# Performance work log

Hardware: AMD Instinct MI355X
Metric: run time of the kernel (lower is better)

## Reference

```python
import jax, jax.numpy as jnp
import numpy as np
from jax import lax

B, S, D = 4, 128, 256
POOL = 3


def conv_block(x, w, b, stride, pool_k):
    # x: (N, Cin, H, W), w: (Cout, Cin, kh, kw)
    y = lax.conv_general_dilated(
        x, w, window_strides=(stride, stride), padding='VALID',
        dimension_numbers=('NCHW', 'OIHW', 'NCHW'))
    y = y + b[None, :, None, None]
    y = jax.nn.gelu(y, approximate=False)  # torch GELU default is exact
    # MaxPool2d(kernel_size=pool_k) -> stride = pool_k, VALID
    y = lax.reduce_window(y, -jnp.inf, lax.max,
                          (1, 1, pool_k, pool_k), (1, 1, pool_k, pool_k), 'VALID')
    return y


def setup_inputs() -> dict:
    key = jax.random.key(0)
    ks = jax.random.split(key, 8)
    token_features = jax.random.normal(ks[0], (B, S, D), dtype=jnp.float32)
    type_embedds = jax.random.normal(ks[1], (B, S, D), dtype=jnp.float32)
    # Conv2dFeatures(depth=3, num_channels=16, start_kernel=3, start_stride=2, pool_kernel=3)
    w1 = jax.random.normal(ks[2], (16, 1, 3, 3), dtype=jnp.float32) * 0.1
    b1 = jax.random.normal(ks[3], (16,), dtype=jnp.float32) * 0.01
    w2 = jax.random.normal(ks[4], (32, 16, 3, 3), dtype=jnp.float32) * 0.05
    b2 = jax.random.normal(ks[5], (32,), dtype=jnp.float32) * 0.01
    w3 = jax.random.normal(ks[6], (32, 32, 3, 3), dtype=jnp.float32) * 0.05
    b3 = jax.random.normal(ks[7], (32,), dtype=jnp.float32) * 0.01
    return dict(token_features=token_features, type_embedds=type_embedds,
                w1=w1, b1=b1, w2=w2, b2=b2, w3=w3, b3=b3)


def reference(token_features, type_embedds, w1, b1, w2, b2, w3, b3):
    b, s, d = type_embedds.shape
    # Outter2dFusion: fused[n,s,i,j] = type_embedds[n,s,i] * token_features[n,s,j]
    fused = jnp.einsum('bsi,bsj->bsij', type_embedds, token_features)
    # Conv stack applied per seq position with in_channels=1 == one batched conv
    x = fused.reshape(b * s, 1, d, d)
    x = conv_block(x, w1, b1, stride=2, pool_k=POOL)
    x = conv_block(x, w2, b2, stride=1, pool_k=POOL)
    x = conv_block(x, w3, b3, stride=1, pool_k=POOL)
    # Dropout is identity in eval mode
    return x.reshape(b, s, -1)
```

## Files before the change

### kernel.cpp

```cpp
#include <hip/hip_runtime.h>
#include <math.h>


#define NIMG 512

__device__ __forceinline__ float gelu_exact(float x) {
    return 0.5f * x * (1.0f + erff(x * 0.70710678118654752f));
}

__device__ __forceinline__ float pool_gelu(float vmin, float vmax) {
    return fmaxf(gelu_exact(vmin), gelu_exact(vmax));
}

__global__ __launch_bounds__(256) void k1_fused(const float* __restrict__ tok,
                                                const float* __restrict__ typ,
                                                const float* __restrict__ w1,
                                                const float* __restrict__ b1,
                                                float* __restrict__ s1) {
    const int blk = blockIdx.x;
    const int img = blk >> 2;
    const int cg  = blk & 3;
    __shared__ float t[256];
    __shared__ float f[256];
    __shared__ float g[4][3][128];

    const int tid = threadIdx.x;
    t[tid] = typ[img * 256 + tid];
    f[tid] = tok[img * 256 + tid];
    __syncthreads();

    for (int idx = tid; idx < 4 * 3 * 126; idx += 256) {
        const int x  = idx % 126;
        const int di = (idx / 126) % 3;
        const int c  = idx / (126 * 3);
        const int cc = cg * 4 + c;
        float acc = 0.f;
#pragma unroll
        for (int dj = 0; dj < 3; ++dj)
            acc += w1[cc * 9 + di * 3 + dj] * f[2 * x + dj];
        g[c][di][x] = acc;
    }
    __syncthreads();

    for (int idx = tid; idx < 4 * 42 * 42; idx += 256) {
        const int px = idx % 42;
        const int py = (idx / 42) % 42;
        const int c  = idx / (42 * 42);
        const int cc = cg * 4 + c;
        float vmin = INFINITY, vmax = -INFINITY;
#pragma unroll
        for (int wy = 0; wy < 3; ++wy) {
            const int y = 3 * py + wy;
            const float t0 = t[2 * y], t1 = t[2 * y + 1], t2 = t[2 * y + 2];
#pragma unroll
            for (int wx = 0; wx < 3; ++wx) {
                const int x = 3 * px + wx;
                const float v = t0 * g[c][0][x] + t1 * g[c][1][x] + t2 * g[c][2][x];
                vmin = fminf(vmin, v);
                vmax = fmaxf(vmax, v);
            }
        }
        const float bias = b1[cc];
        s1[((img * 16 + cc) * 42 + py) * 42 + px] = pool_gelu(vmin + bias, vmax + bias);
    }
}

__global__ __launch_bounds__(256) void k2_conv(const float* __restrict__ s1,
                                               const float* __restrict__ w2,
                                               const float* __restrict__ b2,
                                               float* __restrict__ s2) {
    const int blk = blockIdx.x;
    const int img = blk >> 2;
    const int cog = blk & 3;
    __shared__ float4 slab4[441];
    __shared__ float wl[8 * 16 * 9];
    float* slab = (float*)slab4;

    const int tid  = threadIdx.x;
    const int lane = tid & 63;
    const int grp  = tid >> 6;
    const int co_l0 = grp;
    const int co_l1 = grp + 4;

    for (int i = tid; i < 8 * 16 * 9; i += 256) wl[i] = w2[cog * 8 * 16 * 9 + i];

    int base[3], valid[3], py[3], px[3];
#pragma unroll
    for (int tI = 0; tI < 3; ++tI) {
        const int c = lane + 64 * tI;
        valid[tI] = (c < 169);
        const int cc = valid[tI] ? c : 168;
        py[tI] = cc % 13;
        px[tI] = cc / 13;
        base[tI] = py[tI] * 126 + px[tI] * 3;
    }

    float acc[2][3][9];
#pragma unroll
    for (int a = 0; a < 2; ++a)
#pragma unroll
        for (int tI = 0; tI < 3; ++tI)
#pragma unroll
            for (int k = 0; k < 9; ++k) acc[a][tI][k] = 0.f;

    const float* s1img = s1 + (size_t)img * 16 * 1764;

    for (int cin = 0; cin < 16; ++cin) {
        __syncthreads();
        const float4* src = (const float4*)(s1img + cin * 1764);
        for (int i = tid; i < 441; i += 256) slab4[i] = src[i];
        __syncthreads();

        float w0[9], w1r[9];
#pragma unroll
        for (int k = 0; k < 9; ++k) {
            w0[k]  = wl[(co_l0 * 16 + cin) * 9 + k];
            w1r[k] = wl[(co_l1 * 16 + cin) * 9 + k];
        }

#pragma unroll
        for (int tI = 0; tI < 3; ++tI) {
            float win[5][5];
#pragma unroll
            for (int r = 0; r < 5; ++r)
#pragma unroll
                for (int c2 = 0; c2 < 5; ++c2)
                    win[r][c2] = slab[base[tI] + r * 42 + c2];
#pragma unroll
            for (int wy = 0; wy < 3; ++wy)
#pragma unroll
                for (int wx = 0; wx < 3; ++wx) {
#pragma unroll
                    for (int dy = 0; dy < 3; ++dy)
#pragma unroll
                        for (int dx = 0; dx < 3; ++dx) {
                            const float v = win[wy + dy][wx + dx];
                            acc[0][tI][wy * 3 + wx] += v * w0[dy * 3 + dx];
                            acc[1][tI][wy * 3 + wx] += v * w1r[dy * 3 + dx];
                        }
                }
        }
    }

    const float b0 = b2[cog * 8 + co_l0];
    const float b1 = b2[cog * 8 + co_l1];
#pragma unroll
    for (int tI = 0; tI < 3; ++tI) {
        if (valid[tI]) {
#pragma unroll
            for (int a = 0; a < 2; ++a) {
                float vmin = INFINITY, vmax = -INFINITY;
#pragma unroll
                for (int k = 0; k < 9; ++k) {
                    vmin = fminf(vmin, acc[a][tI][k]);
                    vmax = fmaxf(vmax, acc[a][tI][k]);
                }
                const float bias = a ? b1 : b0;
                const int co = cog * 8 + (a ? co_l1 : co_l0);
                s2[((img * 32 + co) * 13 + py[tI]) * 13 + px[tI]] =
                    pool_gelu(vmin + bias, vmax + bias);
            }
        }
    }
}

__global__ __launch_bounds__(320) void k3_conv(const float* __restrict__ s2,
                                               const float* __restrict__ w3,
                                               const float* __restrict__ b3,
                                               float* __restrict__ out) {
    const int img = blockIdx.x;
    __shared__ float4 s2l4[1352];
    __shared__ float4 wl4[2304];
    float* s2l = (float*)s2l4;
    float* wl  = (float*)wl4;

    const int tid = threadIdx.x;
    const float4* src = (const float4*)(s2 + (size_t)img * 5408);
    for (int i = tid; i < 1352; i += 320) s2l4[i] = src[i];
    const float4* wsrc = (const float4*)w3;
    for (int i = tid; i < 2304; i += 320) wl4[i] = wsrc[i];
    __syncthreads();

    if (tid < 288) {
        const int co   = tid / 9;
        const int cell = tid % 9;
        const int cy = cell / 3, cx = cell % 3;
        const int base = (3 * cy) * 13 + 3 * cx;

        float acc[9];
#pragma unroll
        for (int k = 0; k < 9; ++k) acc[k] = 0.f;

        for (int cin = 0; cin < 32; ++cin) {
            float w[9];
#pragma unroll
            for (int k = 0; k < 9; ++k) w[k] = wl[(co * 32 + cin) * 9 + k];
            float win[5][5];
#pragma unroll
            for (int r = 0; r < 5; ++r)
#pragma unroll
                for (int c2 = 0; c2 < 5; ++c2)
                    win[r][c2] = s2l[cin * 169 + base + r * 13 + c2];
#pragma unroll
            for (int wy = 0; wy < 3; ++wy)
#pragma unroll
                for (int wx = 0; wx < 3; ++wx)
#pragma unroll
                    for (int dy = 0; dy < 3; ++dy)
#pragma unroll
                        for (int dx = 0; dx < 3; ++dx)
                            acc[wy * 3 + wx] += win[wy + dy][wx + dx] * w[dy * 3 + dx];
        }

        float vmin = INFINITY, vmax = -INFINITY;
#pragma unroll
        for (int k = 0; k < 9; ++k) {
            vmin = fminf(vmin, acc[k]);
            vmax = fmaxf(vmax, acc[k]);
        }
        const float bias = b3[co];
        out[(size_t)img * 288 + tid] = pool_gelu(vmin + bias, vmax + bias);
    }
}

extern "C" void kernel_launch(void* const* d_in, const int* in_sizes, int n_in,
                              void* d_out, int out_size, void* d_ws, size_t ws_size,
                              hipStream_t stream) {
    const float* tok = (const float*)d_in[0];
    const float* typ = (const float*)d_in[1];
    const float* w1  = (const float*)d_in[2];
    const float* b1  = (const float*)d_in[3];
    const float* w2  = (const float*)d_in[4];
    const float* b2  = (const float*)d_in[5];
    const float* w3  = (const float*)d_in[6];
    const float* b3  = (const float*)d_in[7];
    float* out = (float*)d_out;

    float* s1 = (float*)d_ws;
    float* s2 = s1 + (size_t)NIMG * 16 * 42 * 42;

    k1_fused<<<dim3(NIMG * 4), dim3(256), 0, stream>>>(tok, typ, w1, b1, s1);
    k2_conv<<<dim3(NIMG * 4), dim3(256), 0, stream>>>(s1, w2, b2, s2);
    k3_conv<<<dim3(NIMG), dim3(320), 0, stream>>>(s2, w3, b3, out);
}
```

Before: 296.1 us.

## Restructure conv kernels for register reuse, padded rows, and more outputs per thread

k1 is rewritten so each thread holds one channel's weights and precomputed column products in registers, then walks pooled rows, writing s1 with a padded 44-wide row stride. k2 now computes 4 output channels per thread (16 per block, half as many blocks), loading weights straight from global through a wave-uniform index instead of staging them in LDS. k3 computes 2 output channels per thread with fewer threads. The aim is to cut redundant slab loads and LDS traffic per FMA. The cost is higher register pressure and lower occupancy or parallelism.

```diff
diff --git a/kernel.cpp b/kernel.cpp
--- a/kernel.cpp
+++ b/kernel.cpp
@@ -7,7 +7,6 @@
 __device__ __forceinline__ float gelu_exact(float x) {
     return 0.5f * x * (1.0f + erff(x * 0.70710678118654752f));
 }
-
 __device__ __forceinline__ float pool_gelu(float vmin, float vmax) {
     return fmaxf(gelu_exact(vmin), gelu_exact(vmax));
 }
@@ -18,50 +17,61 @@
                                                 const float* __restrict__ b1,
                                                 float* __restrict__ s1) {
     const int blk = blockIdx.x;
-    const int img = blk >> 2;
-    const int cg  = blk & 3;
-    __shared__ float t[256];
-    __shared__ float f[256];
-    __shared__ float g[4][3][128];
-
+    const int img = blk >> 1;
+    const int py0 = (blk & 1) * 21;
     const int tid = threadIdx.x;
-    t[tid] = typ[img * 256 + tid];
-    f[tid] = tok[img * 256 + tid];
-    __syncthreads();
-
-    for (int idx = tid; idx < 4 * 3 * 126; idx += 256) {
-        const int x  = idx % 126;
-        const int di = (idx / 126) % 3;
-        const int c  = idx / (126 * 3);
-        const int cc = cg * 4 + c;
-        float acc = 0.f;
-#pragma unroll
-        for (int dj = 0; dj < 3; ++dj)
-            acc += w1[cc * 9 + di * 3 + dj] * f[2 * x + dj];
-        g[c][di][x] = acc;
-    }
-    __syncthreads();
-
-    for (int idx = tid; idx < 4 * 42 * 42; idx += 256) {
-        const int px = idx % 42;
-        const int py = (idx / 42) % 42;
-        const int c  = idx / (42 * 42);
-        const int cc = cg * 4 + c;
-        float vmin = INFINITY, vmax = -INFINITY;
-#pragma unroll
-        for (int wy = 0; wy < 3; ++wy) {
-            const int y = 3 * py + wy;
-            const float t0 = t[2 * y], t1 = t[2 * y + 1], t2 = t[2 * y + 2];
-#pragma unroll
-            for (int wx = 0; wx < 3; ++wx) {
-                const int x = 3 * px + wx;
-                const float v = t0 * g[c][0][x] + t1 * g[c][1][x] + t2 * g[c][2][x];
-                vmin = fminf(vmin, v);
-                vmax = fmaxf(vmax, v);
-            }
-        }
-        const float bias = b1[cc];
-        s1[((img * 16 + cc) * 42 + py) * 42 + px] = pool_gelu(vmin + bias, vmax + bias);
+    const int c     = tid >> 4;
+    const int pslot = tid & 15;
+
+    float wv[9];
+#pragma unroll
+    for (int k = 0; k < 9; ++k) wv[k] = w1[c * 9 + k];
+    const float bias = b1[c];
+
+    const float* frow = tok + img * 256;
+    const float* trow = typ + img * 256;
+
+    float g[3][3][3];
+    int pxv[3];
+#pragma unroll
+    for (int s = 0; s < 3; ++s) {
+        const int px = pslot + 16 * s;
+        pxv[s] = px;
+        const int pe = px < 42 ? px : 41;
+        float f7[7];
+#pragma unroll
+        for (int q = 0; q < 7; ++q) f7[q] = frow[6 * pe + q];
+#pragma unroll
+        for (int di = 0; di < 3; ++di)
+#pragma unroll
+            for (int wx = 0; wx < 3; ++wx)
+                g[s][di][wx] = wv[di * 3 + 0] * f7[2 * wx]
+                             + wv[di * 3 + 1] * f7[2 * wx + 1]
+                             + wv[di * 3 + 2] * f7[2 * wx + 2];
+    }
+
+    float* orow = s1 + ((size_t)img * 16 + c) * (42 * 44);
+    for (int py = py0; py < py0 + 21; ++py) {
+        float ts[7];
+#pragma unroll
+        for (int q = 0; q < 7; ++q) ts[q] = trow[6 * py + q];
+#pragma unroll
+        for (int s = 0; s < 3; ++s) {
+            float vmin = INFINITY, vmax = -INFINITY;
+#pragma unroll
+            for (int wy = 0; wy < 3; ++wy) {
+#pragma unroll
+                for (int wx = 0; wx < 3; ++wx) {
+                    float v = ts[2 * wy] * g[s][0][wx];
+                    v = fmaf(ts[2 * wy + 1], g[s][1][wx], v);
+                    v = fmaf(ts[2 * wy + 2], g[s][2][wx], v);
+                    vmin = fminf(vmin, v);
+                    vmax = fmaxf(vmax, v);
+                }
+            }
+            if (pxv[s] < 42)
+                orow[py * 44 + pxv[s]] = pool_gelu(vmin + bias, vmax + bias);
+        }
     }
 }
 
@@ -70,53 +80,48 @@
                                                const float* __restrict__ b2,
                                                float* __restrict__ s2) {
     const int blk = blockIdx.x;
-    const int img = blk >> 2;
-    const int cog = blk & 3;
-    __shared__ float4 slab4[441];
-    __shared__ float wl[8 * 16 * 9];
+    const int img = blk >> 1;
+    const int cog = blk & 1;
+    __shared__ float4 slab4[462];
     float* slab = (float*)slab4;
 
     const int tid  = threadIdx.x;
     const int lane = tid & 63;
     const int grp  = tid >> 6;
-    const int co_l0 = grp;
-    const int co_l1 = grp + 4;
-
-    for (int i = tid; i < 8 * 16 * 9; i += 256) wl[i] = w2[cog * 8 * 16 * 9 + i];
 
     int base[3], valid[3], py[3], px[3];
 #pragma unroll
     for (int tI = 0; tI < 3; ++tI) {
-        const int c = lane + 64 * tI;
-        valid[tI] = (c < 169);
-        const int cc = valid[tI] ? c : 168;
+        const int cc0 = lane + 64 * tI;
+        valid[tI] = (cc0 < 169);
+        const int cc = valid[tI] ? cc0 : 168;
         py[tI] = cc % 13;
         px[tI] = cc / 13;
-        base[tI] = py[tI] * 126 + px[tI] * 3;
-    }
-
-    float acc[2][3][9];
-#pragma unroll
-    for (int a = 0; a < 2; ++a)
+        base[tI] = py[tI] * 132 + px[tI] * 3;
+    }
+
+    float acc[4][3][9];
+#pragma unroll
+    for (int a = 0; a < 4; ++a)
 #pragma unroll
         for (int tI = 0; tI < 3; ++tI)
 #pragma unroll
             for (int k = 0; k < 9; ++k) acc[a][tI][k] = 0.f;
 
-    const float* s1img = s1 + (size_t)img * 16 * 1764;
+    const float* s1img = s1 + (size_t)img * 16 * 1848;
 
     for (int cin = 0; cin < 16; ++cin) {
         __syncthreads();
-        const float4* src = (const float4*)(s1img + cin * 1764);
-        for (int i = tid; i < 441; i += 256) slab4[i] = src[i];
+        const float4* src = (const float4*)(s1img + cin * 1848);
+        for (int i = tid; i < 462; i += 256) slab4[i] = src[i];
         __syncthreads();
 
-        float w0[9], w1r[9];
-#pragma unroll
-        for (int k = 0; k < 9; ++k) {
-            w0[k]  = wl[(co_l0 * 16 + cin) * 9 + k];
-            w1r[k] = wl[(co_l1 * 16 + cin) * 9 + k];
-        }
+        const int wbase = __builtin_amdgcn_readfirstlane((cog * 16 + grp) * 144 + cin * 9);
+        float wv[4][9];
+#pragma unroll
+        for (int a = 0; a < 4; ++a)
+#pragma unroll
+            for (int k = 0; k < 9; ++k) wv[a][k] = w2[wbase + a * 576 + k];
 
 #pragma unroll
         for (int tI = 0; tI < 3; ++tI) {
@@ -125,82 +130,85 @@
             for (int r = 0; r < 5; ++r)
 #pragma unroll
                 for (int c2 = 0; c2 < 5; ++c2)
-                    win[r][c2] = slab[base[tI] + r * 42 + c2];
+                    win[r][c2] = slab[base[tI] + r * 44 + c2];
 #pragma unroll
             for (int wy = 0; wy < 3; ++wy)
 #pragma unroll
-                for (int wx = 0; wx < 3; ++wx) {
+                for (int wx = 0; wx < 3; ++wx)
 #pragma unroll
                     for (int dy = 0; dy < 3; ++dy)
 #pragma unroll
                         for (int dx = 0; dx < 3; ++dx) {
                             const float v = win[wy + dy][wx + dx];
-                            acc[0][tI][wy * 3 + wx] += v * w0[dy * 3 + dx];
-                            acc[1][tI][wy * 3 + wx] += v * w1r[dy * 3 + dx];
+#pragma unroll
+                            for (int a = 0; a < 4; ++a)
+                                acc[a][tI][wy * 3 + wx] =
+                                    fmaf(v, wv[a][dy * 3 + dx], acc[a][tI][wy * 3 + wx]);
                         }
-                }
-        }
-    }
-
-    const float b0 = b2[cog * 8 + co_l0];
-    const float b1 = b2[cog * 8 + co_l1];
+        }
+    }
+
 #pragma unroll
     for (int tI = 0; tI < 3; ++tI) {
         if (valid[tI]) {
 #pragma unroll
-            for (int a = 0; a < 2; ++a) {
+            for (int a = 0; a < 4; ++a) {
                 float vmin = INFINITY, vmax = -INFINITY;
 #pragma unroll
                 for (int k = 0; k < 9; ++k) {
                     vmin = fminf(vmin, acc[a][tI][k]);
                     vmax = fmaxf(vmax, acc[a][tI][k]);
                 }
-                const float bias = a ? b1 : b0;
-                const int co = cog * 8 + (a ? co_l1 : co_l0);
+                const int co = cog * 16 + grp + 4 * a;
+                const float b = b2[co];
                 s2[((img * 32 + co) * 13 + py[tI]) * 13 + px[tI]] =
-                    pool_gelu(vmin + bias, vmax + bias);
-            }
-        }
-    }
-}
-
-__global__ __launch_bounds__(320) void k3_conv(const float* __restrict__ s2,
+                    pool_gelu(vmin + b, vmax + b);
+            }
+        }
+    }
+}
+
+__global__ __launch_bounds__(192) void k3_conv(const float* __restrict__ s2,
                                                const float* __restrict__ w3,
                                                const float* __restrict__ b3,
                                                float* __restrict__ out) {
     const int img = blockIdx.x;
     __shared__ float4 s2l4[1352];
-    __shared__ float4 wl4[2304];
+    __shared__ float wl[32 * 32 * 9];
     float* s2l = (float*)s2l4;
-    float* wl  = (float*)wl4;
 
     const int tid = threadIdx.x;
     const float4* src = (const float4*)(s2 + (size_t)img * 5408);
-    for (int i = tid; i < 1352; i += 320) s2l4[i] = src[i];
-    const float4* wsrc = (const float4*)w3;
-    for (int i = tid; i < 2304; i += 320) wl4[i] = wsrc[i];
+    for (int i = tid; i < 1352; i += 192) s2l4[i] = src[i];
+    for (int i = tid; i < 9216; i += 192) wl[i] = w3[i];
     __syncthreads();
 
-    if (tid < 288) {
-        const int co   = tid / 9;
+    if (tid < 144) {
+        const int cp   = tid / 9;
         const int cell = tid % 9;
         const int cy = cell / 3, cx = cell % 3;
         const int base = (3 * cy) * 13 + 3 * cx;
-
-        float acc[9];
-#pragma unroll
-        for (int k = 0; k < 9; ++k) acc[k] = 0.f;
+        const int co0 = 2 * cp, co1 = 2 * cp + 1;
+
+        float acc[2][9];
+#pragma unroll
+        for (int a = 0; a < 2; ++a)
+#pragma unroll
+            for (int k = 0; k < 9; ++k) acc[a][k] = 0.f;
 
         for (int cin = 0; cin < 32; ++cin) {
-            float w[9];
-#pragma unroll
-            for (int k = 0; k < 9; ++k) w[k] = wl[(co * 32 + cin) * 9 + k];
             float win[5][5];
 #pragma unroll
             for (int r = 0; r < 5; ++r)
 #pragma unroll
                 for (int c2 = 0; c2 < 5; ++c2)
                     win[r][c2] = s2l[cin * 169 + base + r * 13 + c2];
+            float wk[2][9];
+#pragma unroll
+            for (int k = 0; k < 9; ++k) {
+                wk[0][k] = wl[(co0 * 32 + cin) * 9 + k];
+                wk[1][k] = wl[(co1 * 32 + cin) * 9 + k];
+            }
 #pragma unroll
             for (int wy = 0; wy < 3; ++wy)
 #pragma unroll
@@ -208,18 +216,25 @@
 #pragma unroll
                     for (int dy = 0; dy < 3; ++dy)
 #pragma unroll
-                        for (int dx = 0; dx < 3; ++dx)
-                            acc[wy * 3 + wx] += win[wy + dy][wx + dx] * w[dy * 3 + dx];
-        }
-
-        float vmin = INFINITY, vmax = -INFINITY;
-#pragma unroll
-        for (int k = 0; k < 9; ++k) {
-            vmin = fminf(vmin, acc[k]);
-            vmax = fmaxf(vmax, acc[k]);
-        }
-        const float bias = b3[co];
-        out[(size_t)img * 288 + tid] = pool_gelu(vmin + bias, vmax + bias);
+                        for (int dx = 0; dx < 3; ++dx) {
+                            const float v = win[wy + dy][wx + dx];
+                            acc[0][wy * 3 + wx] = fmaf(v, wk[0][dy * 3 + dx], acc[0][wy * 3 + wx]);
+                            acc[1][wy * 3 + wx] = fmaf(v, wk[1][dy * 3 + dx], acc[1][wy * 3 + wx]);
+                        }
+        }
+
+#pragma unroll
+        for (int a = 0; a < 2; ++a) {
+            float vmin = INFINITY, vmax = -INFINITY;
+#pragma unroll
+            for (int k = 0; k < 9; ++k) {
+                vmin = fminf(vmin, acc[a][k]);
+                vmax = fmaxf(vmax, acc[a][k]);
+            }
+            const int co = a ? co1 : co0;
+            const float b = b3[co];
+            out[(size_t)img * 288 + co * 9 + cell] = pool_gelu(vmin + b, vmax + b);
+        }
     }
 }
 
@@ -237,9 +252,9 @@
     float* out = (float*)d_out;
 
     float* s1 = (float*)d_ws;
-    float* s2 = s1 + (size_t)NIMG * 16 * 42 * 42;
-
-    k1_fused<<<dim3(NIMG * 4), dim3(256), 0, stream>>>(tok, typ, w1, b1, s1);
-    k2_conv<<<dim3(NIMG * 4), dim3(256), 0, stream>>>(s1, w2, b2, s2);
-    k3_conv<<<dim3(NIMG), dim3(320), 0, stream>>>(s2, w3, b3, out);
-}
+    float* s2 = s1 + (size_t)NIMG * 16 * 42 * 44;
+
+    k1_fused<<<dim3(NIMG * 2), dim3(256), 0, stream>>>(tok, typ, w1, b1, s1);
+    k2_conv<<<dim3(NIMG * 2), dim3(256), 0, stream>>>(s1, w2, b2, s2);
+    k3_conv<<<dim3(NIMG), dim3(192), 0, stream>>>(s2, w3, b3, out);
+}
```

Measured after the change: 259.8 us. -12.3%, faster.
